# Kernel optimization log

Hardware: AMD Instinct MI355X
Metric: run time of the kernel (lower is better)

## Reference

```python
import jax, jax.numpy as jnp
import numpy as np

B, C, H, W = 16, 512, 32, 32
COND_C, L_COND = 768, 77
N_GROUPS, N_HEADS = 8, 8
HEAD = C // N_HEADS
EPS = 1e-5


def setup_inputs() -> dict:
    key = jax.random.key(0)
    ks = jax.random.split(key, 6)
    s = lambda fan_in: 1.0 / np.sqrt(fan_in)
    return {
        "x_0": jax.random.normal(ks[0], (B, C, H, W), jnp.float32),
        "cond": jax.random.normal(ks[1], (B, L_COND, COND_C), jnp.float32),
        "gn_gamma": jnp.ones((C,), jnp.float32),
        "gn_beta": jnp.zeros((C,), jnp.float32),
        "qkv_w": jax.random.normal(ks[2], (3 * C, C), jnp.float32) * s(C),
        "qkv_b": jnp.zeros((3 * C,), jnp.float32),
        "cond_kv_w": jax.random.normal(ks[3], (2 * C, COND_C), jnp.float32) * s(COND_C),
        "cond_kv_b": jnp.zeros((2 * C,), jnp.float32),
        "out_w": jax.random.normal(ks[4], (C, C), jnp.float32) * s(C),
        "out_b": jnp.zeros((C,), jnp.float32),
    }


def reference(x_0, cond, gn_gamma, gn_beta, qkv_w, qkv_b, cond_kv_w, cond_kv_b, out_w, out_b):
    b, c, h, w = x_0.shape
    L = h * w
    # --- GroupNorm over (C/G, H, W) per group, per-channel affine ---
    xg = x_0.reshape(b, N_GROUPS, c // N_GROUPS, h * w)
    mu = xg.mean(axis=(2, 3), keepdims=True)
    var = xg.var(axis=(2, 3), keepdims=True)
    xn = ((xg - mu) * jax.lax.rsqrt(var + EPS)).reshape(b, c, h, w)
    xn = xn * gn_gamma[None, :, None, None] + gn_beta[None, :, None, None]
    # --- to tokens [B, L, C] ---
    x = xn.transpose(0, 2, 3, 1).reshape(b, L, c)
    # --- QKV ---
    qkv = x @ qkv_w.T + qkv_b  # [B, L, 3C]
    q, k, v = jnp.split(qkv, 3, axis=-1)
    q = q.reshape(b, L, N_HEADS, HEAD)
    k = k.reshape(b, L, N_HEADS, HEAD)
    v = v.reshape(b, L, N_HEADS, HEAD)
    # --- conditional K/V ---
    kv_c = cond @ cond_kv_w.T + cond_kv_b  # [B, Lc, 2C]
    k_c, v_c = jnp.split(kv_c, 2, axis=-1)
    Lc = cond.shape[1]
    k_c = k_c.reshape(b, Lc, N_HEADS, HEAD)
    v_c = v_c.reshape(b, Lc, N_HEADS, HEAD)
    K = jnp.concatenate([k, k_c], axis=1)  # [B, L+Lc, H, D]
    V = jnp.concatenate([v, v_c], axis=1)
    # --- attention (full score matrix, as in the original) ---
    scale = HEAD ** -0.5
    scores = jnp.einsum("bqhd,bkhd->bhqk", q, K) * scale
    att = jax.nn.softmax(scores, axis=-1)
    out = jnp.einsum("bhqk,bkhd->bqhd", att, V).reshape(b, L, c)
    out = out @ out_w.T + out_b
    # --- back to image + residual ---
    out = out.reshape(b, h, w, c).transpose(0, 3, 1, 2)
    return out + x_0
```

## Files before the change

### kernel.cpp

```cpp
#include <hip/hip_runtime.h>

typedef short bf16x8 __attribute__((ext_vector_type(8)));
typedef float f32x4 __attribute__((ext_vector_type(4)));
typedef float f32x16 __attribute__((ext_vector_type(16)));
typedef unsigned int u32x4 __attribute__((ext_vector_type(4)));

#define KVP 1152

__device__ __forceinline__ unsigned short f2b(float f) {
    unsigned int u = __float_as_uint(f);
    u += 0x7FFFu + ((u >> 16) & 1u);
    return (unsigned short)(u >> 16);
}

__device__ __forceinline__ f32x4 mfma16(bf16x8 a, bf16x8 b, f32x4 c) {
    return __builtin_amdgcn_mfma_f32_16x16x32_bf16(a, b, c, 0, 0, 0);
}
__device__ __forceinline__ f32x16 mfma32(bf16x8 a, bf16x8 b, f32x16 c) {
    return __builtin_amdgcn_mfma_f32_32x32x16_bf16(a, b, c, 0, 0, 0);
}
__device__ __forceinline__ float exp2_raw(float x) {
    float r; asm("v_exp_f32 %0, %1" : "=v"(r) : "v"(x)); return r;
}
__device__ __forceinline__ unsigned cvt_pk(float lo, float hi) {
    unsigned r; asm("v_cvt_pk_bf16_f32 %0, %1, %2" : "=v"(r) : "v"(lo), "v"(hi)); return r;
}
__device__ __forceinline__ float f3(float a, float b, float c) { return fmaxf(fmaxf(a, b), c); }

typedef __attribute__((address_space(3))) unsigned int lds_u32_t;
typedef const __attribute__((address_space(1))) unsigned int glb_u32_t;
__device__ __forceinline__ void async_cp16(const void* g, void* l) {
    __builtin_amdgcn_global_load_lds((glb_u32_t*)(unsigned long long)g,
                                     (lds_u32_t*)(unsigned int)(unsigned long long)l,
                                     16, 0, 0);
}

__global__ __launch_bounds__(256) void prep_k(const float* __restrict__ x, float2* __restrict__ part,
                                              const float* __restrict__ a, unsigned short* __restrict__ oa,
                                              const float* __restrict__ b, unsigned short* __restrict__ ob,
                                              const float* __restrict__ c, unsigned short* __restrict__ oc,
                                              const float* __restrict__ d, unsigned short* __restrict__ od) {
    if (blockIdx.x < 512) {
        int blk = blockIdx.x;
        const float4* p = (const float4*)(x + (size_t)blk * 16384);
        float s = 0.f, ss = 0.f;
        for (int i = threadIdx.x; i < 4096; i += 256) {
            float4 v = p[i];
            s  += v.x + v.y + v.z + v.w;
            ss += v.x * v.x + v.y * v.y + v.z * v.z + v.w * v.w;
        }
#pragma unroll
        for (int o = 32; o; o >>= 1) { s += __shfl_down(s, o); ss += __shfl_down(ss, o); }
        __shared__ float red[8];
        int w = threadIdx.x >> 6;
        if ((threadIdx.x & 63) == 0) { red[w] = s; red[4 + w] = ss; }
        __syncthreads();
        if (threadIdx.x == 0) {
            s  = red[0] + red[1] + red[2] + red[3];
            ss = red[4] + red[5] + red[6] + red[7];
            part[blk] = make_float2(s, ss);
        }
        return;
    }
    int i = (blockIdx.x - 512) * 256 + threadIdx.x;
    const float* src; unsigned short* dst; int j;
    if (i < 196608)      { src = a; dst = oa; j = i; }
    else if (i < 393216) { src = b; dst = ob; j = i - 196608; }
    else if (i < 458752) { src = c; dst = oc; j = i - 393216; }
    else if (i < 695296) { src = d; dst = od; j = i - 458752; }
    else return;
    float4 v = ((const float4*)src)[j];
    uint2 u = make_uint2(cvt_pk(v.x, v.y), cvt_pk(v.z, v.w));
    ((uint2*)dst)[j] = u;
}

__global__ __launch_bounds__(256) void gn_apply_k(const float* __restrict__ x, const float2* __restrict__ part,
                                                  const float* __restrict__ gamma, const float* __restrict__ beta,
                                                  unsigned short* __restrict__ xt) {
    int st = blockIdx.x & 15;
    int ct = (blockIdx.x >> 4) & 7;
    int b  = blockIdx.x >> 7;
    int bg = b * 8 + ct;
    float2 p0 = part[4 * bg], p1 = part[4 * bg + 1], p2 = part[4 * bg + 2], p3 = part[4 * bg + 3];
    float s = (p0.x + p1.x) + (p2.x + p3.x);
    float ss = (p0.y + p1.y) + (p2.y + p3.y);
    float mean = s * (1.f / 65536.f);
    float var  = ss * (1.f / 65536.f) - mean * mean;
    float rsig = rsqrtf(var + 1e-5f);
    __shared__ unsigned short tile[64][65];
    int tid = threadIdx.x;
#pragma unroll
    for (int it = 0; it < 4; ++it) {
        int idx = it * 256 + tid;
        int ci = idx >> 4, j4 = idx & 15;
        int c = ct * 64 + ci;
        float4 v = *(const float4*)(x + ((size_t)b * 512 + c) * 1024 + st * 64 + j4 * 4);
        float gs = gamma[c] * rsig;
        float bo = beta[c] - mean * gs;
        tile[j4 * 4 + 0][ci] = f2b(v.x * gs + bo);
        tile[j4 * 4 + 1][ci] = f2b(v.y * gs + bo);
        tile[j4 * 4 + 2][ci] = f2b(v.z * gs + bo);
        tile[j4 * 4 + 3][ci] = f2b(v.w * gs + bo);
    }
    __syncthreads();
#pragma unroll
    for (int it = 0; it < 4; ++it) {
        int idx = it * 256 + tid;
        int si = idx >> 4, q = idx & 15;
        uint2 u;
        u.x = (unsigned)tile[si][q * 4 + 0] | ((unsigned)tile[si][q * 4 + 1] << 16);
        u.y = (unsigned)tile[si][q * 4 + 2] | ((unsigned)tile[si][q * 4 + 3] << 16);
        *(uint2*)(xt + ((size_t)b * 1024 + st * 64 + si) * 512 + ct * 64 + q * 4) = u;
    }
}

template <int EPI>
__global__ __launch_bounds__(512) void gemm256_k(const unsigned short* __restrict__ A,
                                                 const unsigned short* __restrict__ Bw,
                                                 const float* __restrict__ bias,
                                                 int K,
                                                 unsigned short* __restrict__ Qo,
                                                 unsigned short* __restrict__ Ko,
                                                 unsigned short* __restrict__ Vo,
                                                 const float* __restrict__ x0,
                                                 float* __restrict__ outp) {
    __shared__ __align__(16) unsigned short As[3][8192];
    __shared__ __align__(16) unsigned short Bs[3][4096];
    const int m0 = blockIdx.x * 256, n0 = blockIdx.y * 128;
    const bool swp = (EPI == 0) && (blockIdx.y < 8);
    const int tid = threadIdx.x, lane = tid & 63, w = tid >> 6;
    const int wr = w >> 1, wc = w & 1;
    const int lc = lane & 15, lg = lane >> 4;

    const int sRow = lane >> 2;
    const int sSlot = (lane & 3) ^ ((lane >> 3) & 3);
    const unsigned short* aSrc0 = A + (size_t)(m0 + 16 * w + sRow) * K + sSlot * 8;
    const unsigned short* aSrc1 = A + (size_t)(m0 + 128 + 16 * w + sRow) * K + sSlot * 8;
    const unsigned short* bSrc0 = Bw + (size_t)(n0 + 16 * w + sRow) * K + sSlot * 8;

    const int rSlot8 = (lg ^ ((lc >> 1) & 3)) * 8;

    f32x4 acc[4][4];
#pragma unroll
    for (int m = 0; m < 4; ++m)
#pragma unroll
        for (int n = 0; n < 4; ++n) acc[m][n] = (f32x4){0.f, 0.f, 0.f, 0.f};

    const int nT = K >> 5;
    async_cp16(aSrc0, &As[0][w * 512]);
    async_cp16(aSrc1, &As[0][(8 + w) * 512]);
    async_cp16(bSrc0, &Bs[0][w * 512]);
    async_cp16(aSrc0 + 32, &As[1][w * 512]);
    async_cp16(aSrc1 + 32, &As[1][(8 + w) * 512]);
    async_cp16(bSrc0 + 32, &Bs[1][w * 512]);

    int c = 0;
#pragma unroll 1
    for (int t = 0; t < nT; ++t) {
        if (t + 2 < nT) {
            int c2 = c + 2; if (c2 >= 3) c2 -= 3;
            const int k2 = (t + 2) << 5;
            async_cp16(aSrc0 + k2, &As[c2][w * 512]);
            async_cp16(aSrc1 + k2, &As[c2][(8 + w) * 512]);
            async_cp16(bSrc0 + k2, &Bs[c2][w * 512]);
            asm volatile("s_waitcnt vmcnt(6)" ::: "memory");
        } else if (t + 1 < nT) {
            asm volatile("s_waitcnt vmcnt(3)" ::: "memory");
        } else {
            asm volatile("s_waitcnt vmcnt(0)" ::: "memory");
        }
        __builtin_amdgcn_s_barrier();

        bf16x8 af[4], bfr[4];
#pragma unroll
        for (int m = 0; m < 4; ++m)
            af[m] = *(const bf16x8*)&As[c][(wr * 64 + m * 16 + lc) * 32 + rSlot8];
#pragma unroll
        for (int n = 0; n < 4; ++n)
            bfr[n] = *(const bf16x8*)&Bs[c][(wc * 64 + n * 16 + lc) * 32 + rSlot8];

        __builtin_amdgcn_s_setprio(1);
        if (swp) {
#pragma unroll
            for (int m = 0; m < 4; ++m)
#pragma unroll
                for (int n = 0; n < 4; ++n)
                    acc[m][n] = mfma16(bfr[n], af[m], acc[m][n]);
        } else {
#pragma unroll
            for (int m = 0; m < 4; ++m)
#pragma unroll
                for (int n = 0; n < 4; ++n)
                    acc[m][n] = mfma16(af[m], bfr[n], acc[m][n]);
        }
        __builtin_amdgcn_s_setprio(0);
        __builtin_amdgcn_s_barrier();

        ++c; if (c == 3) c = 0;
    }

    if (EPI == 0) {
        if (swp) {
            const bool isQ = (n0 < 512);
            const float sc = isQ ? (0.125f * 1.44269504089f) : 1.f;
#pragma unroll
            for (int n = 0; n < 4; ++n) {
                const int c0 = n0 + wc * 64 + n * 16 + lg * 4;
                const float4 b4 = *(const float4*)&bias[c0];
#pragma unroll
                for (int m = 0; m < 4; ++m) {
                    const int tok = m0 + wr * 64 + m * 16 + lc;
                    const int b = tok >> 10, l = tok & 1023;
                    float v0 = (acc[m][n][0] + b4.x) * sc;
                    float v1 = (acc[m][n][1] + b4.y) * sc;
                    float v2 = (acc[m][n][2] + b4.z) * sc;
                    float v3 = (acc[m][n][3] + b4.w) * sc;
                    uint2 u = make_uint2(cvt_pk(v0, v1), cvt_pk(v2, v3));
                    if (isQ) {
                        const int hh = c0 >> 6, d = c0 & 63;
                        *(uint2*)(Qo + ((size_t)(b * 8 + hh) * 1024 + l) * 64 + d) = u;
                    } else {
                        const int hh = (c0 - 512) >> 6, d = c0 & 63;
                        *(uint2*)(Ko + ((size_t)(b * 8 + hh) * KVP + l) * 64 + d) = u;
                    }
                }
            }
        } else {
#pragma unroll
            for (int n = 0; n < 4; ++n) {
                const int col = n0 + wc * 64 + n * 16 + lc;
                const int j = col - 1024;
                const int hh = j >> 6, d = j & 63;
                const float bv = bias[col];
#pragma unroll
                for (int m = 0; m < 4; ++m) {
                    const int t0 = m0 + wr * 64 + m * 16 + lg * 4;
                    const int b = t0 >> 10, l0 = t0 & 1023;
                    uint2 u = make_uint2(cvt_pk(acc[m][n][0] + bv, acc[m][n][1] + bv),
                                         cvt_pk(acc[m][n][2] + bv, acc[m][n][3] + bv));
                    *(uint2*)(Vo + ((size_t)(b * 8 + hh) * 64 + d) * KVP + l0) = u;
                }
            }
        }
    } else {
#pragma unroll
        for (int n = 0; n < 4; ++n) {
            const int col = n0 + wc * 64 + n * 16 + lc;
            const float bv = bias[col];
#pragma unroll
            for (int m = 0; m < 4; ++m) {
                const int t0 = m0 + wr * 64 + m * 16 + lg * 4;
                const size_t a = ((size_t)(t0 >> 10) * 512 + col) * 1024 + (t0 & 1023);
                float4 xv = *(const float4*)(x0 + a);
                float4 o;
                o.x = acc[m][n][0] + bv + xv.x;
                o.y = acc[m][n][1] + bv + xv.y;
                o.z = acc[m][n][2] + bv + xv.z;
                o.w = acc[m][n][3] + bv + xv.w;
                *(float4*)(outp + a) = o;
            }
        }
    }
}

__global__ __launch_bounds__(256) void gemm_nt_k(const unsigned short* __restrict__ A,
                                                 const unsigned short* __restrict__ Bw,
                                                 const float* __restrict__ bias,
                                                 int M, int N, int K,
                                                 unsigned short* __restrict__ Ko,
                                                 unsigned short* __restrict__ Vo) {
    __shared__ unsigned short As[64][40];
    __shared__ unsigned short Bs[64][40];
    const int m0 = blockIdx.x * 64, n0 = blockIdx.y * 64;
    const int tid = threadIdx.x, lane = tid & 63, w = tid >> 6;
    const int lc = lane & 15, lg = lane >> 4;
    const int lrow = tid >> 2, lseg = tid & 3;
    f32x4 acc[4];
#pragma unroll
    for (int i = 0; i < 4; ++i) acc[i] = (f32x4){0.f, 0.f, 0.f, 0.f};

    for (int k0 = 0; k0 < K; k0 += 32) {
        uint4 av = make_uint4(0u, 0u, 0u, 0u);
        if (m0 + lrow < M) av = *(const uint4*)(A + (size_t)(m0 + lrow) * K + k0 + lseg * 8);
        *(uint4*)&As[lrow][lseg * 8] = av;
        uint4 bv = *(const uint4*)(Bw + (size_t)(n0 + lrow) * K + k0 + lseg * 8);
        *(uint4*)&Bs[lrow][lseg * 8] = bv;
        __syncthreads();
        bf16x8 af = *(const bf16x8*)&As[w * 16 + lc][lg * 8];
#pragma unroll
        for (int ct = 0; ct < 4; ++ct) {
            bf16x8 bfr = *(const bf16x8*)&Bs[ct * 16 + lc][lg * 8];
            acc[ct] = mfma16(af, bfr, acc[ct]);
        }
        __syncthreads();
    }

    const int rbase = m0 + w * 16 + lg * 4;
#pragma unroll
    for (int ct = 0; ct < 4; ++ct) {
        int col = n0 + ct * 16 + lc;
        float bv = bias[col];
#pragma unroll
        for (int r = 0; r < 4; ++r) {
            int token = rbase + r;
            if (token >= M) continue;
            float val = acc[ct][r] + bv;
            int b = token / 77, l = token - b * 77;
            if (col < 512) {
                int hh = col >> 6, d = col & 63;
                Ko[((size_t)(b * 8 + hh) * KVP + 1024 + l) * 64 + d] = f2b(val);
            } else {
                int j = col - 512, hh = j >> 6, d = j & 63;
                Vo[((size_t)(b * 8 + hh) * 64 + d) * KVP + 1024 + l] = f2b(val);
            }
        }
    }
}

__global__ __launch_bounds__(512) void attn2_k(const unsigned short* __restrict__ Q,
                                               const unsigned short* __restrict__ Kb,
                                               const unsigned short* __restrict__ Vt,
                                               unsigned short* __restrict__ atok) {
    __shared__ __align__(16) unsigned short lds[18432];

    const int bid = blockIdx.x;
    const int bh = bid & 127;
    const int qt = bid >> 7;
    const int w  = threadIdx.x >> 6;
    const int lane = threadIdx.x & 63;
    const int ql = lane & 31, hi = lane >> 5;
    const int q0 = qt * 256 + w * 32;

    bf16x8 qf[4];
    const unsigned short* Qp = Q + ((size_t)bh * 1024 + q0 + ql) * 64 + hi * 8;
#pragma unroll
    for (int ks = 0; ks < 4; ++ks) qf[ks] = *(const bf16x8*)(Qp + ks * 16);

    const unsigned short* Kg = Kb + (size_t)bh * KVP * 64;
    const unsigned short* Vg = Vt + (size_t)bh * 64 * KVP;

    const int srow = lane >> 3;
    const int sc   = (((lane & 7) ^ (lane >> 3)) << 3);

    f32x16 o0, o1;
#pragma unroll
    for (int i = 0; i < 16; ++i) { o0[i] = 0.f; o1[i] = 0.f; }
    float mreg = -1e30f, lsum = 0.f;

    {
        uint4 kr = *(const uint4*)(Kg + (size_t)(8 * w + srow) * 64 + sc);
        uint4 vr = *(const uint4*)(Vg + (size_t)(8 * w + srow) * KVP + sc);
        *(uint4*)&lds[w * 512 + lane * 8] = kr;
        *(uint4*)&lds[4096 + w * 512 + lane * 8] = vr;
    }
    __syncthreads();

    int cur = 0;
    for (int it = 0; it < 18; ++it) {
        const int kv0 = it * 64;
        const bool pre = (it < 17);
        uint4 kn, vn;
        if (pre) {
            kn = *(const uint4*)(Kg + (size_t)(kv0 + 64 + 8 * w + srow) * 64 + sc);
            vn = *(const uint4*)(Vg + (size_t)(8 * w + srow) * KVP + kv0 + 64 + sc);
        }
        const int kb = cur * 8192, vb = cur * 8192 + 4096;

        f32x16 s0, s1;
#pragma unroll
        for (int i = 0; i < 16; ++i) { s0[i] = 0.f; s1[i] = 0.f; }
        __builtin_amdgcn_s_setprio(1);
#pragma unroll
        for (int ks = 0; ks < 4; ++ks) {
            const int sl = ((ks * 2 + hi) ^ (ql & 7)) << 3;
            bf16x8 kf0 = *(const bf16x8*)&lds[kb + ql * 64 + sl];
            bf16x8 kf1 = *(const bf16x8*)&lds[kb + (32 + ql) * 64 + sl];
            s0 = mfma32(kf0, qf[ks], s0);
            s1 = mfma32(kf1, qf[ks], s1);
        }
        __builtin_amdgcn_s_setprio(0);
        if (kv0 == 1088) {
#pragma unroll
            for (int r = 0; r < 16; ++r) {
                int kva = 1088 + (r & 3) + 8 * (r >> 2) + 4 * hi;
                if (kva >= 1101) s0[r] = -1e30f;
                if (kva + 32 >= 1101) s1[r] = -1e30f;
            }
        }

        float t[16];
#pragma unroll
        for (int i = 0; i < 16; ++i) t[i] = fmaxf(s0[i], s1[i]);
        float a0m = f3(t[0], t[1], t[2]),  a1m = f3(t[3], t[4], t[5]);
        float a2m = f3(t[6], t[7], t[8]),  a3m = f3(t[9], t[10], t[11]);
        float a4m = f3(t[12], t[13], t[14]);
        float pm  = fmaxf(f3(a0m, a1m, a2m), f3(a3m, a4m, t[15]));
        float pmax = fmaxf(pm, __shfl_xor(pm, 32));

        if (__any(pmax > mreg + 8.f)) {
            float mn = fmaxf(mreg, pmax);
            float al = exp2_raw(mreg - mn);
            mreg = mn;
            lsum *= al;
#pragma unroll
            for (int i = 0; i < 16; ++i) { o0[i] *= al; o1[i] *= al; }
        }

        unsigned pk0[8], pk1[8];
        float sA = 0.f, sB = 0.f, sC = 0.f, sD = 0.f;
#pragma unroll
        for (int i = 0; i < 8; ++i) {
            float a0 = exp2_raw(s0[2 * i] - mreg), a1 = exp2_raw(s0[2 * i + 1] - mreg);
            float b0 = exp2_raw(s1[2 * i] - mreg), b1 = exp2_raw(s1[2 * i + 1] - mreg);
            pk0[i] = cvt_pk(a0, a1);
            pk1[i] = cvt_pk(b0, b1);
            sA += a0; sB += a1; sC += b0; sD += b1;
        }
        float ls = (sA + sB) + (sC + sD);
        ls += __shfl_xor(ls, 32);
        lsum += ls;

#pragma unroll
        for (int t2 = 0; t2 < 2; ++t2) {
            const unsigned* pk = t2 ? pk1 : pk0;
#pragma unroll
            for (int v = 0; v < 2; ++v) {
                unsigned a0 = pk[4 * v], a1 = pk[4 * v + 1], a2 = pk[4 * v + 2], a3 = pk[4 * v + 3];
                unsigned x = __shfl_xor(hi ? a0 : a2, 32);
                unsigned y = __shfl_xor(hi ? a1 : a3, 32);
                u32x4 fw;
                fw.x = hi ? x : a0; fw.y = hi ? y : a1; fw.z = hi ? a2 : x; fw.w = hi ? a3 : y;
                bf16x8 pf = __builtin_bit_cast(bf16x8, fw);
                const int ks2 = 2 * t2 + v;
                const int sl = ((ks2 * 2 + hi) ^ (ql & 7)) << 3;
                bf16x8 vf0 = *(const bf16x8*)&lds[vb + ql * 64 + sl];
                bf16x8 vf1 = *(const bf16x8*)&lds[vb + (32 + ql) * 64 + sl];
                __builtin_amdgcn_s_setprio(1);
                o0 = mfma32(vf0, pf, o0);
                o1 = mfma32(vf1, pf, o1);
                __builtin_amdgcn_s_setprio(0);
            }
        }

        if (pre) {
            *(uint4*)&lds[(cur ^ 1) * 8192 + w * 512 + lane * 8] = kn;
            *(uint4*)&lds[(cur ^ 1) * 8192 + 4096 + w * 512 + lane * 8] = vn;
        }
        __syncthreads();
        cur ^= 1;
    }

    float rinv = 1.f / lsum;
    unsigned short* sw = &lds[w * 2304];
#pragma unroll
    for (int dt = 0; dt < 2; ++dt) {
#pragma unroll
        for (int rp = 0; rp < 8; ++rp) {
            float e0 = (dt ? o1[2 * rp] : o0[2 * rp]) * rinv;
            float e1 = (dt ? o1[2 * rp + 1] : o0[2 * rp + 1]) * rinv;
            int d = dt * 32 + ((2 * rp) & 3) + 8 * ((2 * rp) >> 2) + 4 * hi;
            *(unsigned*)&sw[ql * 72 + d] = cvt_pk(e0, e1);
        }
    }
    __syncthreads();
    {
        int i = threadIdx.x >> 1, hf = threadIdx.x & 1;
        const unsigned short* src = &lds[(i >> 5) * 2304 + (i & 31) * 72 + hf * 32];
        u32x4 r0 = *(const u32x4*)(src);
        u32x4 r1 = *(const u32x4*)(src + 8);
        u32x4 r2 = *(const u32x4*)(src + 16);
        u32x4 r3 = *(const u32x4*)(src + 24);
        int b = bh >> 3, h = bh & 7;
        unsigned short* gd = atok + ((size_t)b * 1024 + qt * 256 + i) * 512 + h * 64 + hf * 32;
        *(u32x4*)(gd) = r0;
        *(u32x4*)(gd + 8) = r1;
        *(u32x4*)(gd + 16) = r2;
        *(u32x4*)(gd + 24) = r3;
    }
}

extern "C" void kernel_launch(void* const* d_in, const int* in_sizes, int n_in,
                              void* d_out, int out_size, void* d_ws, size_t ws_size,
                              hipStream_t stream) {
    const float* x0     = (const float*)d_in[0];
    const float* cond   = (const float*)d_in[1];
    const float* gamma  = (const float*)d_in[2];
    const float* beta   = (const float*)d_in[3];
    const float* qkv_w  = (const float*)d_in[4];
    const float* qkv_b  = (const float*)d_in[5];
    const float* ckv_w  = (const float*)d_in[6];
    const float* ckv_b  = (const float*)d_in[7];
    const float* out_w  = (const float*)d_in[8];
    const float* out_b  = (const float*)d_in[9];
    float* outp = (float*)d_out;

    char* p = (char*)d_ws;
    float2* part = (float2*)p;           p += 4096;
    unsigned short* xt    = (unsigned short*)p; p += (size_t)16384 * 512 * 2;
    unsigned short* wqkv  = (unsigned short*)p; p += (size_t)1536 * 512 * 2;
    unsigned short* wckv  = (unsigned short*)p; p += (size_t)1024 * 768 * 2;
    unsigned short* wout  = (unsigned short*)p; p += (size_t)512 * 512 * 2;
    unsigned short* condb = (unsigned short*)p; p += (size_t)1232 * 768 * 2;
    unsigned short* Qb    = (unsigned short*)p; p += (size_t)16 * 8 * 1024 * 64 * 2;
    unsigned short* Kb    = (unsigned short*)p; p += (size_t)16 * 8 * KVP * 64 * 2;
    unsigned short* Vtb   = (unsigned short*)p; p += (size_t)16 * 8 * KVP * 64 * 2;
    unsigned short* atok  = (unsigned short*)p; p += (size_t)16384 * 512 * 2;

    prep_k<<<512 + 2716, 256, 0, stream>>>(x0, part, qkv_w, wqkv, ckv_w, wckv, out_w, wout, cond, condb);
    gn_apply_k<<<2048, 256, 0, stream>>>(x0, part, gamma, beta, xt);

    gemm256_k<0><<<dim3(64, 12), 512, 0, stream>>>(xt, wqkv, qkv_b, 512,
                                                   Qb, Kb, Vtb, nullptr, nullptr);
    gemm_nt_k<<<dim3(20, 16), 256, 0, stream>>>(condb, wckv, ckv_b, 1232, 1024, 768, Kb, Vtb);
    attn2_k<<<512, 512, 0, stream>>>(Qb, Kb, Vtb, atok);
    gemm256_k<2><<<dim3(64, 4), 512, 0, stream>>>(atok, wout, out_b, 512,
                                                  nullptr, nullptr, nullptr, x0, outp);
}
```

Measured before the change: 174.4 us.

## Widen GEMM K-tile to 64 with 8-slot XOR swizzle and single-stage prefetch

The 256x128 GEMM kernel now stages 64-wide K slices instead of 32, using a new 8-way XOR swizzle for the LDS layout. Each main-loop iteration runs two MFMA sub-steps on the staged slice. Prefetch distance drops from two tiles to one, still with three LDS buffers, which lets the trailing barrier be removed. The aim is to halve the number of loop iterations and barriers per GEMM. The cost is LDS use rising to roughly 144 KB per block, which likely limits each CU to one resident block, and less latency hiding from the shorter prefetch distance.

```diff
diff --git a/kernel.cpp b/kernel.cpp
--- a/kernel.cpp
+++ b/kernel.cpp
@@ -124,21 +124,18 @@
                                                  unsigned short* __restrict__ Vo,
                                                  const float* __restrict__ x0,
                                                  float* __restrict__ outp) {
-    __shared__ __align__(16) unsigned short As[3][8192];
-    __shared__ __align__(16) unsigned short Bs[3][4096];
+    __shared__ __align__(16) unsigned short As[3][256 * 64];
+    __shared__ __align__(16) unsigned short Bs[3][128 * 64];
     const int m0 = blockIdx.x * 256, n0 = blockIdx.y * 128;
     const bool swp = (EPI == 0) && (blockIdx.y < 8);
     const int tid = threadIdx.x, lane = tid & 63, w = tid >> 6;
     const int wr = w >> 1, wc = w & 1;
     const int lc = lane & 15, lg = lane >> 4;
 
-    const int sRow = lane >> 2;
-    const int sSlot = (lane & 3) ^ ((lane >> 3) & 3);
-    const unsigned short* aSrc0 = A + (size_t)(m0 + 16 * w + sRow) * K + sSlot * 8;
-    const unsigned short* aSrc1 = A + (size_t)(m0 + 128 + 16 * w + sRow) * K + sSlot * 8;
-    const unsigned short* bSrc0 = Bw + (size_t)(n0 + 16 * w + sRow) * K + sSlot * 8;
-
-    const int rSlot8 = (lg ^ ((lc >> 1) & 3)) * 8;
+    const int r8 = lane >> 3;
+    const int sSw = ((lane & 7) ^ (r8 & 7)) * 8;
+    const unsigned short* aS = A + (size_t)(m0 + w * 32 + r8) * K + sSw;
+    const unsigned short* bS = Bw + (size_t)(n0 + w * 16 + r8) * K + sSw;
 
     f32x4 acc[4][4];
 #pragma unroll
@@ -146,58 +143,66 @@
 #pragma unroll
         for (int n = 0; n < 4; ++n) acc[m][n] = (f32x4){0.f, 0.f, 0.f, 0.f};
 
-    const int nT = K >> 5;
-    async_cp16(aSrc0, &As[0][w * 512]);
-    async_cp16(aSrc1, &As[0][(8 + w) * 512]);
-    async_cp16(bSrc0, &Bs[0][w * 512]);
-    async_cp16(aSrc0 + 32, &As[1][w * 512]);
-    async_cp16(aSrc1 + 32, &As[1][(8 + w) * 512]);
-    async_cp16(bSrc0 + 32, &Bs[1][w * 512]);
+    const int nT = K >> 6;
+
+#define STAGE64(tile, buf)                                                             \
+    {                                                                                  \
+        const int k0_ = (tile) << 6;                                                   \
+        async_cp16(aS + k0_,                    &As[buf][(w * 32) * 64]);              \
+        async_cp16(aS + k0_ + (size_t)8 * K,    &As[buf][(w * 32 + 8) * 64]);          \
+        async_cp16(aS + k0_ + (size_t)16 * K,   &As[buf][(w * 32 + 16) * 64]);         \
+        async_cp16(aS + k0_ + (size_t)24 * K,   &As[buf][(w * 32 + 24) * 64]);         \
+        async_cp16(bS + k0_,                    &Bs[buf][(w * 16) * 64]);              \
+        async_cp16(bS + k0_ + (size_t)8 * K,    &Bs[buf][(w * 16 + 8) * 64]);          \
+    }
+
+    STAGE64(0, 0);
 
     int c = 0;
 #pragma unroll 1
     for (int t = 0; t < nT; ++t) {
-        if (t + 2 < nT) {
-            int c2 = c + 2; if (c2 >= 3) c2 -= 3;
-            const int k2 = (t + 2) << 5;
-            async_cp16(aSrc0 + k2, &As[c2][w * 512]);
-            async_cp16(aSrc1 + k2, &As[c2][(8 + w) * 512]);
-            async_cp16(bSrc0 + k2, &Bs[c2][w * 512]);
+        if (t + 1 < nT) {
+            int c1 = c + 1; if (c1 == 3) c1 = 0;
+            STAGE64(t + 1, c1);
             asm volatile("s_waitcnt vmcnt(6)" ::: "memory");
-        } else if (t + 1 < nT) {
-            asm volatile("s_waitcnt vmcnt(3)" ::: "memory");
         } else {
             asm volatile("s_waitcnt vmcnt(0)" ::: "memory");
         }
         __builtin_amdgcn_s_barrier();
 
-        bf16x8 af[4], bfr[4];
-#pragma unroll
-        for (int m = 0; m < 4; ++m)
-            af[m] = *(const bf16x8*)&As[c][(wr * 64 + m * 16 + lc) * 32 + rSlot8];
-#pragma unroll
-        for (int n = 0; n < 4; ++n)
-            bfr[n] = *(const bf16x8*)&Bs[c][(wc * 64 + n * 16 + lc) * 32 + rSlot8];
-
-        __builtin_amdgcn_s_setprio(1);
-        if (swp) {
-#pragma unroll
-            for (int m = 0; m < 4; ++m)
-#pragma unroll
-                for (int n = 0; n < 4; ++n)
-                    acc[m][n] = mfma16(bfr[n], af[m], acc[m][n]);
-        } else {
-#pragma unroll
-            for (int m = 0; m < 4; ++m)
-#pragma unroll
-                for (int n = 0; n < 4; ++n)
-                    acc[m][n] = mfma16(af[m], bfr[n], acc[m][n]);
-        }
-        __builtin_amdgcn_s_setprio(0);
-        __builtin_amdgcn_s_barrier();
+#pragma unroll
+        for (int kk = 0; kk < 2; ++kk) {
+            bf16x8 af[4], bfr[4];
+#pragma unroll
+            for (int m = 0; m < 4; ++m) {
+                const int row = wr * 64 + m * 16 + lc;
+                af[m] = *(const bf16x8*)&As[c][row * 64 + (((kk * 4 + lg) ^ (lc & 7)) * 8)];
+            }
+#pragma unroll
+            for (int n = 0; n < 4; ++n) {
+                const int row = wc * 64 + n * 16 + lc;
+                bfr[n] = *(const bf16x8*)&Bs[c][row * 64 + (((kk * 4 + lg) ^ (lc & 7)) * 8)];
+            }
+            __builtin_amdgcn_s_setprio(1);
+            if (swp) {
+#pragma unroll
+                for (int m = 0; m < 4; ++m)
+#pragma unroll
+                    for (int n = 0; n < 4; ++n)
+                        acc[m][n] = mfma16(bfr[n], af[m], acc[m][n]);
+            } else {
+#pragma unroll
+                for (int m = 0; m < 4; ++m)
+#pragma unroll
+                    for (int n = 0; n < 4; ++n)
+                        acc[m][n] = mfma16(af[m], bfr[n], acc[m][n]);
+            }
+            __builtin_amdgcn_s_setprio(0);
+        }
 
         ++c; if (c == 3) c = 0;
     }
+#undef STAGE64
 
     if (EPI == 0) {
         if (swp) {
```

Measured after the change: 167.0 us (median of 3 runs). -4.2%, faster.

## Enlarge GEMM tiles to 256x256 and switch to single-barrier triple-buffered prefetch

Applied to the files above, without the earlier changes.

The shared GEMM kernel's output tile grows from 256x128 to 256x256, so each warp computes a 128x64 subtile (8x4 MFMA fragments). This raises data reuse per LDS load and halves the grid for the QKV and output projections. The K-loop now prefetches only one tile ahead into a three-buffer ring and drops the trailing barrier, leaving one barrier per iteration. In exchange the blocks need twice the accumulators and more LDS, and the smaller grid (384 and 128 blocks) may underfill the 256 CUs, especially for the output projection.

```diff
diff --git a/kernel.cpp b/kernel.cpp
--- a/kernel.cpp
+++ b/kernel.cpp
@@ -125,79 +125,78 @@
                                                  const float* __restrict__ x0,
                                                  float* __restrict__ outp) {
     __shared__ __align__(16) unsigned short As[3][8192];
-    __shared__ __align__(16) unsigned short Bs[3][4096];
-    const int m0 = blockIdx.x * 256, n0 = blockIdx.y * 128;
-    const bool swp = (EPI == 0) && (blockIdx.y < 8);
+    __shared__ __align__(16) unsigned short Bs[3][8192];
+    const int m0 = blockIdx.x * 256, n0 = blockIdx.y * 256;
+    const bool swp = (EPI == 0) && (blockIdx.y < 4);
     const int tid = threadIdx.x, lane = tid & 63, w = tid >> 6;
-    const int wr = w >> 1, wc = w & 1;
+    const int wM = w >> 2, wN = w & 3;
     const int lc = lane & 15, lg = lane >> 4;
 
     const int sRow = lane >> 2;
     const int sSlot = (lane & 3) ^ ((lane >> 3) & 3);
-    const unsigned short* aSrc0 = A + (size_t)(m0 + 16 * w + sRow) * K + sSlot * 8;
-    const unsigned short* aSrc1 = A + (size_t)(m0 + 128 + 16 * w + sRow) * K + sSlot * 8;
-    const unsigned short* bSrc0 = Bw + (size_t)(n0 + 16 * w + sRow) * K + sSlot * 8;
+    const unsigned short* aS = A + (size_t)(m0 + 32 * w + sRow) * K + sSlot * 8;
+    const unsigned short* bS = Bw + (size_t)(n0 + 32 * w + sRow) * K + sSlot * 8;
 
     const int rSlot8 = (lg ^ ((lc >> 1) & 3)) * 8;
 
-    f32x4 acc[4][4];
-#pragma unroll
-    for (int m = 0; m < 4; ++m)
+    f32x4 acc[8][4];
+#pragma unroll
+    for (int m = 0; m < 8; ++m)
 #pragma unroll
         for (int n = 0; n < 4; ++n) acc[m][n] = (f32x4){0.f, 0.f, 0.f, 0.f};
 
     const int nT = K >> 5;
-    async_cp16(aSrc0, &As[0][w * 512]);
-    async_cp16(aSrc1, &As[0][(8 + w) * 512]);
-    async_cp16(bSrc0, &Bs[0][w * 512]);
-    async_cp16(aSrc0 + 32, &As[1][w * 512]);
-    async_cp16(aSrc1 + 32, &As[1][(8 + w) * 512]);
-    async_cp16(bSrc0 + 32, &Bs[1][w * 512]);
+
+#define STAGE32(tile, buf)                                                       \
+    {                                                                            \
+        const int k0_ = (tile) << 5;                                             \
+        async_cp16(aS + k0_,                  &As[buf][(32 * w) * 32]);          \
+        async_cp16(aS + k0_ + (size_t)16 * K, &As[buf][(32 * w + 16) * 32]);     \
+        async_cp16(bS + k0_,                  &Bs[buf][(32 * w) * 32]);          \
+        async_cp16(bS + k0_ + (size_t)16 * K, &Bs[buf][(32 * w + 16) * 32]);     \
+    }
+
+    STAGE32(0, 0);
 
     int c = 0;
 #pragma unroll 1
     for (int t = 0; t < nT; ++t) {
-        if (t + 2 < nT) {
-            int c2 = c + 2; if (c2 >= 3) c2 -= 3;
-            const int k2 = (t + 2) << 5;
-            async_cp16(aSrc0 + k2, &As[c2][w * 512]);
-            async_cp16(aSrc1 + k2, &As[c2][(8 + w) * 512]);
-            async_cp16(bSrc0 + k2, &Bs[c2][w * 512]);
-            asm volatile("s_waitcnt vmcnt(6)" ::: "memory");
-        } else if (t + 1 < nT) {
-            asm volatile("s_waitcnt vmcnt(3)" ::: "memory");
+        if (t + 1 < nT) {
+            int c1 = c + 1; if (c1 == 3) c1 = 0;
+            STAGE32(t + 1, c1);
+            asm volatile("s_waitcnt vmcnt(4)" ::: "memory");
         } else {
             asm volatile("s_waitcnt vmcnt(0)" ::: "memory");
         }
         __builtin_amdgcn_s_barrier();
 
-        bf16x8 af[4], bfr[4];
-#pragma unroll
-        for (int m = 0; m < 4; ++m)
-            af[m] = *(const bf16x8*)&As[c][(wr * 64 + m * 16 + lc) * 32 + rSlot8];
+        bf16x8 af[8], bfr[4];
+#pragma unroll
+        for (int m = 0; m < 8; ++m)
+            af[m] = *(const bf16x8*)&As[c][(wM * 128 + m * 16 + lc) * 32 + rSlot8];
 #pragma unroll
         for (int n = 0; n < 4; ++n)
-            bfr[n] = *(const bf16x8*)&Bs[c][(wc * 64 + n * 16 + lc) * 32 + rSlot8];
+            bfr[n] = *(const bf16x8*)&Bs[c][(wN * 64 + n * 16 + lc) * 32 + rSlot8];
 
         __builtin_amdgcn_s_setprio(1);
         if (swp) {
 #pragma unroll
-            for (int m = 0; m < 4; ++m)
+            for (int m = 0; m < 8; ++m)
 #pragma unroll
                 for (int n = 0; n < 4; ++n)
                     acc[m][n] = mfma16(bfr[n], af[m], acc[m][n]);
         } else {
 #pragma unroll
-            for (int m = 0; m < 4; ++m)
+            for (int m = 0; m < 8; ++m)
 #pragma unroll
                 for (int n = 0; n < 4; ++n)
                     acc[m][n] = mfma16(af[m], bfr[n], acc[m][n]);
         }
         __builtin_amdgcn_s_setprio(0);
-        __builtin_amdgcn_s_barrier();
 
         ++c; if (c == 3) c = 0;
     }
+#undef STAGE32
 
     if (EPI == 0) {
         if (swp) {
@@ -205,11 +204,11 @@
             const float sc = isQ ? (0.125f * 1.44269504089f) : 1.f;
 #pragma unroll
             for (int n = 0; n < 4; ++n) {
-                const int c0 = n0 + wc * 64 + n * 16 + lg * 4;
+                const int c0 = n0 + wN * 64 + n * 16 + lg * 4;
                 const float4 b4 = *(const float4*)&bias[c0];
 #pragma unroll
-                for (int m = 0; m < 4; ++m) {
-                    const int tok = m0 + wr * 64 + m * 16 + lc;
+                for (int m = 0; m < 8; ++m) {
+                    const int tok = m0 + wM * 128 + m * 16 + lc;
                     const int b = tok >> 10, l = tok & 1023;
                     float v0 = (acc[m][n][0] + b4.x) * sc;
                     float v1 = (acc[m][n][1] + b4.y) * sc;
@@ -228,13 +227,13 @@
         } else {
 #pragma unroll
             for (int n = 0; n < 4; ++n) {
-                const int col = n0 + wc * 64 + n * 16 + lc;
+                const int col = n0 + wN * 64 + n * 16 + lc;
                 const int j = col - 1024;
                 const int hh = j >> 6, d = j & 63;
                 const float bv = bias[col];
 #pragma unroll
-                for (int m = 0; m < 4; ++m) {
-                    const int t0 = m0 + wr * 64 + m * 16 + lg * 4;
+                for (int m = 0; m < 8; ++m) {
+                    const int t0 = m0 + wM * 128 + m * 16 + lg * 4;
                     const int b = t0 >> 10, l0 = t0 & 1023;
                     uint2 u = make_uint2(cvt_pk(acc[m][n][0] + bv, acc[m][n][1] + bv),
                                          cvt_pk(acc[m][n][2] + bv, acc[m][n][3] + bv));
@@ -245,11 +244,11 @@
     } else {
 #pragma unroll
         for (int n = 0; n < 4; ++n) {
-            const int col = n0 + wc * 64 + n * 16 + lc;
+            const int col = n0 + wN * 64 + n * 16 + lc;
             const float bv = bias[col];
 #pragma unroll
-            for (int m = 0; m < 4; ++m) {
-                const int t0 = m0 + wr * 64 + m * 16 + lg * 4;
+            for (int m = 0; m < 8; ++m) {
+                const int t0 = m0 + wM * 128 + m * 16 + lg * 4;
                 const size_t a = ((size_t)(t0 >> 10) * 512 + col) * 1024 + (t0 & 1023);
                 float4 xv = *(const float4*)(x0 + a);
                 float4 o;
@@ -509,10 +508,10 @@
     prep_k<<<512 + 2716, 256, 0, stream>>>(x0, part, qkv_w, wqkv, ckv_w, wckv, out_w, wout, cond, condb);
     gn_apply_k<<<2048, 256, 0, stream>>>(x0, part, gamma, beta, xt);
 
-    gemm256_k<0><<<dim3(64, 12), 512, 0, stream>>>(xt, wqkv, qkv_b, 512,
-                                                   Qb, Kb, Vtb, nullptr, nullptr);
+    gemm256_k<0><<<dim3(64, 6), 512, 0, stream>>>(xt, wqkv, qkv_b, 512,
+                                                  Qb, Kb, Vtb, nullptr, nullptr);
     gemm_nt_k<<<dim3(20, 16), 256, 0, stream>>>(condb, wckv, ckv_b, 1232, 1024, 768, Kb, Vtb);
     attn2_k<<<512, 512, 0, stream>>>(Qb, Kb, Vtb, atok);
-    gemm256_k<2><<<dim3(64, 4), 512, 0, stream>>>(atok, wout, out_b, 512,
+    gemm256_k<2><<<dim3(64, 2), 512, 0, stream>>>(atok, wout, out_b, 512,
                                                   nullptr, nullptr, nullptr, x0, outp);
 }
```

Result: slower. 492.3 us (+182.4%).
